# Optimization experiments

Hardware: AMD Instinct MI355X
Metric: run time of the kernel (lower is better)

## Reference

```python
import jax, jax.numpy as jnp
import numpy as np

TEMP = 0.5  # init temperature
EPS = 1e-12  # F.normalize eps


def setup_inputs() -> dict:
    key = jax.random.key(0)
    k1, k2 = jax.random.split(key)
    batch_embedding = jax.random.normal(k1, (4096, 256), dtype=jnp.float32)
    labels = jax.random.randint(k2, (4096,), 0, 512, dtype=jnp.int64)
    return {"batch_embedding": batch_embedding, "labels": labels}


def reference(batch_embedding, labels):
    n = labels.shape[0]
    dt = batch_embedding.dtype
    # row-normalize; cosine_similarity of normalized rows == norm @ norm.T
    nrm = jnp.linalg.norm(batch_embedding, axis=1, keepdims=True)
    norm = batch_embedding / jnp.maximum(nrm, EPS)
    sim = norm @ norm.T  # [n, n]
    mask = (labels[:, None] == labels[None, :]).astype(dt)  # same-label pairs (incl. diagonal)
    eye = jnp.eye(n, dtype=dt)
    exp_sim = jnp.exp(sim / TEMP) * (1.0 - eye)  # zero diagonal
    pos = mask * exp_sim
    neg_sum = jnp.sum(exp_sim - pos, axis=1)  # per-row negative sum
    ratio = pos / (pos + neg_sum[:, None])
    loss_mat = -jnp.log((1.0 - mask) + ratio + eye)
    nnz = jnp.count_nonzero(loss_mat).astype(dt)
    return jnp.sum(loss_mat) / nnz
```

## Files before the change

### kernel.cpp

```cpp
#include <hip/hip_runtime.h>
#include <hip/hip_bf16.h>


#define N_ROWS 4096
#define K_DIM  256

typedef __attribute__((ext_vector_type(4))) float float4v;
typedef __attribute__((ext_vector_type(4))) float f4;
typedef __attribute__((ext_vector_type(4))) int   int4v;
typedef __attribute__((ext_vector_type(2))) long  long2v;

#define PK_OFF    0
#define PART_OFF  (2 * 1024 * 1024)
#define ACC_OFF   (PART_OFF + 4 * 64 * N_ROWS * 4)

__device__ __forceinline__ void gll16(const void* g, void* l) {
    __builtin_amdgcn_global_load_lds(
        (const __attribute__((address_space(1))) unsigned int*)g,
        (__attribute__((address_space(3))) unsigned int*)l, 16, 0, 0);
}

__global__ void normalize_kernel(const float* __restrict__ emb,
                                 unsigned char* __restrict__ pk8,
                                 float* __restrict__ acc) {
    int tile = blockIdx.x, t = threadIdx.x;
    __shared__ float lds[16 * 256];
    __shared__ float sc[16];
    const f4* src = (const f4*)(emb + tile * 16 * 256);
    f4* dst4 = (f4*)lds;
    #pragma unroll
    for (int it = 0; it < 4; ++it) dst4[t + 256 * it] = src[t + 256 * it];
    __syncthreads();
    int wave = t >> 6, lane = t & 63;
    int row = wave * 4 + (lane >> 4);
    float s = 0.f;
    #pragma unroll
    for (int m = 0; m < 16; ++m) {
        float x = lds[row * 256 + (lane & 15) + 16 * m];
        s += x * x;
    }
    s += __shfl_xor(s, 1); s += __shfl_xor(s, 2);
    s += __shfl_xor(s, 4); s += __shfl_xor(s, 8);
    float scale = 1.0f / fmaxf(sqrtf(s), 1e-12f);
    if ((lane & 15) == 0) sc[row] = scale;
    __syncthreads();
    int u = t >> 6, quad = (t >> 4) & 3, r16 = t & 15;
    float s8 = sc[r16] * 8.0f;
    const float* lr = lds + r16 * 256;
    int4v wv;
    #pragma unroll
    for (int wi = 0; wi < 4; ++wi) {
        int h  = wi >> 1;
        int j0 = (wi & 1) * 4;
        int kb = quad * 8 + (2 * u + h) * 32 + j0;
        float v0 = lr[kb + 0] * s8, v1 = lr[kb + 1] * s8;
        float v2 = lr[kb + 2] * s8, v3 = lr[kb + 3] * s8;
        int wd = __builtin_amdgcn_cvt_pk_fp8_f32(v0, v1, 0, 0);
        wd     = __builtin_amdgcn_cvt_pk_fp8_f32(v2, v3, wd, 1);
        wv[wi] = wd;
    }
    *(int4v*)(pk8 + tile * 4096 + t * 16) = wv;
    if (tile == 0 && t < 4) acc[t] = 0.0f;
}

__global__ __launch_bounds__(256, 3)
void negsum_kernel(const unsigned char* __restrict__ pk8,
                   const int* __restrict__ labels,
                   float* __restrict__ part) {
    __shared__ __align__(16) unsigned char Bs8[32768];
    int t = threadIdx.x;
    int w = t >> 6, lane = t & 63;
    int lane16 = lane & 15, quad = lane >> 4;
    int xcd = blockIdx.x & 7, local = blockIdx.x >> 3;
    int bi = xcd * 4 + (local >> 5);
    int bj = local & 31;
    int wi = w >> 1, wj = w & 1;

    int ibase = bi * 128 + wi * 64;
    int jbase = bj * 128 + wj * 64;
    const char* pkb = (const char*)pk8;

    #pragma unroll
    for (int u = 0; u < 8; ++u) {
        int c8 = w * 8 + u, tl = c8 >> 2, cs = c8 & 3;
        gll16(pkb + (((bj * 8 + tl) << 12) | (cs << 10)) + lane * 16,
              Bs8 + (c8 << 10));
    }
    long2v av[4][4];
    #pragma unroll
    for (int it = 0; it < 4; ++it)
        #pragma unroll
        for (int cs = 0; cs < 4; ++cs)
            av[it][cs] = *(const long2v*)(pkb
                + (((bi * 8 + wi * 4 + it) << 12) | (cs << 10)) + lane * 16);

    int labi[16], labj[4];
    #pragma unroll
    for (int it = 0; it < 4; ++it)
        #pragma unroll
        for (int r = 0; r < 4; ++r)
            labi[it * 4 + r] = labels[ibase + it * 16 + quad * 4 + r];
    #pragma unroll
    for (int jt = 0; jt < 4; ++jt)
        labj[jt] = labels[jbase + jt * 16 + lane16];

    float4v acc[4][4];
    #pragma unroll
    for (int a = 0; a < 4; ++a)
        #pragma unroll
        for (int b = 0; b < 4; ++b)
            acc[a][b] = (float4v){0.f, 0.f, 0.f, 0.f};

    __syncthreads();

    #pragma unroll
    for (int cs = 0; cs < 4; ++cs) {
        long2v bv[4];
        #pragma unroll
        for (int jt = 0; jt < 4; ++jt)
            bv[jt] = *(const long2v*)(Bs8
                     + (((((wj * 4 + jt) << 2) | cs) << 10)) + lane * 16);
        #pragma unroll
        for (int h = 0; h < 2; ++h)
            #pragma unroll
            for (int it = 0; it < 4; ++it)
                #pragma unroll
                for (int jt = 0; jt < 4; ++jt)
                    acc[it][jt] = __builtin_amdgcn_mfma_f32_16x16x32_fp8_fp8(
                        av[it][cs][h], bv[jt][h], acc[it][jt], 0, 0, 0);
    }

    float ex[4] = {0,0,0,0}, pe[4] = {0,0,0,0};
    float tt[4] = {0,0,0,0}, pc[4] = {0,0,0,0};
    #pragma unroll
    for (int it = 0; it < 4; ++it) {
        #pragma unroll
        for (int jt = 0; jt < 4; ++jt) {
            int j = jbase + jt * 16 + lane16;
            #pragma unroll
            for (int r = 0; r < 4; ++r) {
                int i = ibase + it * 16 + quad * 4 + r;
                float t2 = acc[it][jt][r] * 0.03125f;
                float e  = __expf(t2);
                bool keep = (i != j);
                bool same = (labi[it * 4 + r] == labj[jt]);
                ex[jt] += keep ? e : 0.0f;
                float m = (same && keep) ? 1.0f : 0.0f;
                pe[jt] = fmaf(m, e,  pe[jt]);
                tt[jt] = fmaf(m, t2, tt[jt]);
                pc[jt] += m;
            }
        }
    }
    int i64 = bi * 2 + wi;
    #pragma unroll
    for (int jt = 0; jt < 4; ++jt) {
        float v0 = ex[jt], v1 = pe[jt], v2 = tt[jt], v3 = pc[jt];
        v0 += __shfl_xor(v0, 16); v0 += __shfl_xor(v0, 32);
        v1 += __shfl_xor(v1, 16); v1 += __shfl_xor(v1, 32);
        v2 += __shfl_xor(v2, 16); v2 += __shfl_xor(v2, 32);
        v3 += __shfl_xor(v3, 16); v3 += __shfl_xor(v3, 32);
        if (quad == 0) {
            int col = jbase + jt * 16 + lane16;
            part[((0 * 64 + i64) << 12) + col] = v0;
            part[((1 * 64 + i64) << 12) + col] = v1;
            part[((2 * 64 + i64) << 12) + col] = v2;
            part[((3 * 64 + i64) << 12) + col] = v3;
        }
    }
}

__global__ void rowreduce_kernel(const float* __restrict__ part,
                                 float* __restrict__ acc,
                                 float* __restrict__ out) {
    int t = threadIdx.x;
    int rl = t & 31, sl = t >> 5;
    int row = blockIdx.x * 32 + rl;
    float s[4];
    #pragma unroll
    for (int st = 0; st < 4; ++st) {
        float v = 0.f;
        #pragma unroll
        for (int c = 0; c < 8; ++c)
            v += part[((st * 64 + (sl * 8 + c)) << 12) + row];
        s[st] = v;
    }
    #pragma unroll
    for (int st = 0; st < 4; ++st) s[st] += __shfl_xor(s[st], 32);
    __shared__ float sred[4][4][32];
    int wave = t >> 6, lane = t & 63;
    if (lane < 32) {
        #pragma unroll
        for (int st = 0; st < 4; ++st) sred[wave][st][lane] = s[st];
    }
    __syncthreads();
    float lsum = 0.f, pcm = 0.f;
    if (t < 32) {
        float tot[4];
        #pragma unroll
        for (int st = 0; st < 4; ++st)
            tot[st] = sred[0][st][t] + sred[1][st][t]
                    + sred[2][st][t] + sred[3][st][t];
        if (tot[3] > 0.f) {
            float n = tot[0] - tot[1];
            lsum = tot[3] * logf(n) + tot[1] / n - tot[2];
            pcm  = tot[3];
        }
    }
    #pragma unroll
    for (int m = 1; m < 32; m <<= 1) {
        lsum += __shfl_xor(lsum, m);
        pcm  += __shfl_xor(pcm,  m);
    }
    if (t == 0) {
        atomicAdd(&acc[0], lsum);
        atomicAdd(&acc[1], pcm);
        __threadfence();
        int ticket = atomicAdd((int*)(acc + 2), 1);
        if (ticket == 127) {
            float ls = atomicAdd(&acc[0], 0.0f);
            float cs = atomicAdd(&acc[1], 0.0f);
            out[0] = ls / cs;
        }
    }
}

extern "C" void kernel_launch(void* const* d_in, const int* in_sizes, int n_in,
                              void* d_out, int out_size, void* d_ws, size_t ws_size,
                              hipStream_t stream) {
    const float* emb    = (const float*)d_in[0];
    const int*   labels = (const int*)d_in[1];
    float* out = (float*)d_out;
    char*  ws  = (char*)d_ws;

    unsigned char* pk8  = (unsigned char*)(ws + PK_OFF);
    float*         part = (float*)(ws + PART_OFF);
    float*         acc  = (float*)(ws + ACC_OFF);

    normalize_kernel<<<N_ROWS / 16, 256, 0, stream>>>(emb, pk8, acc);
    negsum_kernel<<<1024, 256, 0, stream>>>(pk8, labels, part);
    rowreduce_kernel<<<128, 256, 0, stream>>>(part, acc, out);
}
```

Baseline: 78.52 us.

## Process two column tiles per block and correct diagonal terms in row reduction

Each negsum block now handles two adjacent 128-column tiles, which halves the grid and reuses the A fragments held in registers. The second B tile is loaded into LDS while the first tile's epilogue runs. The per-element diagonal masking is removed from the epilogue. The row reduction instead subtracts the known diagonal contribution (exp(2), 2 and a count of 1), which assumes the diagonal similarity is exactly 1. Under fp8 quantization that self-similarity is only approximately 1, so the result can drift slightly.

```diff
diff --git a/kernel.cpp b/kernel.cpp
--- a/kernel.cpp
+++ b/kernel.cpp
@@ -72,18 +72,18 @@
     int w = t >> 6, lane = t & 63;
     int lane16 = lane & 15, quad = lane >> 4;
     int xcd = blockIdx.x & 7, local = blockIdx.x >> 3;
-    int bi = xcd * 4 + (local >> 5);
-    int bj = local & 31;
+    int bi  = xcd * 4 + (local >> 4);
+    int bjp = local & 15;
+    int bj0 = bjp * 2;
     int wi = w >> 1, wj = w & 1;
 
     int ibase = bi * 128 + wi * 64;
-    int jbase = bj * 128 + wj * 64;
     const char* pkb = (const char*)pk8;
 
     #pragma unroll
     for (int u = 0; u < 8; ++u) {
         int c8 = w * 8 + u, tl = c8 >> 2, cs = c8 & 3;
-        gll16(pkb + (((bj * 8 + tl) << 12) | (cs << 10)) + lane * 16,
+        gll16(pkb + (((bj0 * 8 + tl) << 12) | (cs << 10)) + lane * 16,
               Bs8 + (c8 << 10));
     }
     long2v av[4][4];
@@ -94,80 +94,99 @@
             av[it][cs] = *(const long2v*)(pkb
                 + (((bi * 8 + wi * 4 + it) << 12) | (cs << 10)) + lane * 16);
 
-    int labi[16], labj[4];
+    int labi[16], labj0[4], labj1[4];
     #pragma unroll
     for (int it = 0; it < 4; ++it)
         #pragma unroll
         for (int r = 0; r < 4; ++r)
             labi[it * 4 + r] = labels[ibase + it * 16 + quad * 4 + r];
     #pragma unroll
-    for (int jt = 0; jt < 4; ++jt)
-        labj[jt] = labels[jbase + jt * 16 + lane16];
+    for (int jt = 0; jt < 4; ++jt) {
+        labj0[jt] = labels[bj0 * 128       + wj * 64 + jt * 16 + lane16];
+        labj1[jt] = labels[bj0 * 128 + 128 + wj * 64 + jt * 16 + lane16];
+    }
 
     float4v acc[4][4];
+    int i64 = bi * 2 + wi;
+
+    auto mfma_tile = [&]() {
+        #pragma unroll
+        for (int cs = 0; cs < 4; ++cs) {
+            long2v bv[4];
+            #pragma unroll
+            for (int jt = 0; jt < 4; ++jt)
+                bv[jt] = *(const long2v*)(Bs8
+                         + (((((wj * 4 + jt) << 2) | cs) << 10)) + lane * 16);
+            #pragma unroll
+            for (int h = 0; h < 2; ++h)
+                #pragma unroll
+                for (int it = 0; it < 4; ++it)
+                    #pragma unroll
+                    for (int jt = 0; jt < 4; ++jt)
+                        acc[it][jt] = __builtin_amdgcn_mfma_f32_16x16x32_fp8_fp8(
+                            av[it][cs][h], bv[jt][h], acc[it][jt], 0, 0, 0);
+        }
+    };
+
+    auto epi_tile = [&](int jbase, const int (&labjl)[4]) {
+        float ex[4] = {0,0,0,0}, pe[4] = {0,0,0,0};
+        float tt[4] = {0,0,0,0}, pc[4] = {0,0,0,0};
+        #pragma unroll
+        for (int it = 0; it < 4; ++it) {
+            #pragma unroll
+            for (int jt = 0; jt < 4; ++jt) {
+                #pragma unroll
+                for (int r = 0; r < 4; ++r) {
+                    float t2 = acc[it][jt][r] * 0.03125f;
+                    float e  = __expf(t2);
+                    float m  = (labi[it * 4 + r] == labjl[jt]) ? 1.0f : 0.0f;
+                    ex[jt] += e;
+                    pe[jt] = fmaf(m, e,  pe[jt]);
+                    tt[jt] = fmaf(m, t2, tt[jt]);
+                    pc[jt] += m;
+                }
+            }
+        }
+        #pragma unroll
+        for (int jt = 0; jt < 4; ++jt) {
+            float v0 = ex[jt], v1 = pe[jt], v2 = tt[jt], v3 = pc[jt];
+            v0 += __shfl_xor(v0, 16); v0 += __shfl_xor(v0, 32);
+            v1 += __shfl_xor(v1, 16); v1 += __shfl_xor(v1, 32);
+            v2 += __shfl_xor(v2, 16); v2 += __shfl_xor(v2, 32);
+            v3 += __shfl_xor(v3, 16); v3 += __shfl_xor(v3, 32);
+            if (quad == 0) {
+                int col = jbase + jt * 16 + lane16;
+                part[((0 * 64 + i64) << 12) + col] = v0;
+                part[((1 * 64 + i64) << 12) + col] = v1;
+                part[((2 * 64 + i64) << 12) + col] = v2;
+                part[((3 * 64 + i64) << 12) + col] = v3;
+            }
+        }
+    };
+
     #pragma unroll
     for (int a = 0; a < 4; ++a)
         #pragma unroll
         for (int b = 0; b < 4; ++b)
             acc[a][b] = (float4v){0.f, 0.f, 0.f, 0.f};
-
-    __syncthreads();
-
-    #pragma unroll
-    for (int cs = 0; cs < 4; ++cs) {
-        long2v bv[4];
-        #pragma unroll
-        for (int jt = 0; jt < 4; ++jt)
-            bv[jt] = *(const long2v*)(Bs8
-                     + (((((wj * 4 + jt) << 2) | cs) << 10)) + lane * 16);
-        #pragma unroll
-        for (int h = 0; h < 2; ++h)
-            #pragma unroll
-            for (int it = 0; it < 4; ++it)
-                #pragma unroll
-                for (int jt = 0; jt < 4; ++jt)
-                    acc[it][jt] = __builtin_amdgcn_mfma_f32_16x16x32_fp8_fp8(
-                        av[it][cs][h], bv[jt][h], acc[it][jt], 0, 0, 0);
-    }
-
-    float ex[4] = {0,0,0,0}, pe[4] = {0,0,0,0};
-    float tt[4] = {0,0,0,0}, pc[4] = {0,0,0,0};
-    #pragma unroll
-    for (int it = 0; it < 4; ++it) {
-        #pragma unroll
-        for (int jt = 0; jt < 4; ++jt) {
-            int j = jbase + jt * 16 + lane16;
-            #pragma unroll
-            for (int r = 0; r < 4; ++r) {
-                int i = ibase + it * 16 + quad * 4 + r;
-                float t2 = acc[it][jt][r] * 0.03125f;
-                float e  = __expf(t2);
-                bool keep = (i != j);
-                bool same = (labi[it * 4 + r] == labj[jt]);
-                ex[jt] += keep ? e : 0.0f;
-                float m = (same && keep) ? 1.0f : 0.0f;
-                pe[jt] = fmaf(m, e,  pe[jt]);
-                tt[jt] = fmaf(m, t2, tt[jt]);
-                pc[jt] += m;
-            }
-        }
-    }
-    int i64 = bi * 2 + wi;
-    #pragma unroll
-    for (int jt = 0; jt < 4; ++jt) {
-        float v0 = ex[jt], v1 = pe[jt], v2 = tt[jt], v3 = pc[jt];
-        v0 += __shfl_xor(v0, 16); v0 += __shfl_xor(v0, 32);
-        v1 += __shfl_xor(v1, 16); v1 += __shfl_xor(v1, 32);
-        v2 += __shfl_xor(v2, 16); v2 += __shfl_xor(v2, 32);
-        v3 += __shfl_xor(v3, 16); v3 += __shfl_xor(v3, 32);
-        if (quad == 0) {
-            int col = jbase + jt * 16 + lane16;
-            part[((0 * 64 + i64) << 12) + col] = v0;
-            part[((1 * 64 + i64) << 12) + col] = v1;
-            part[((2 * 64 + i64) << 12) + col] = v2;
-            part[((3 * 64 + i64) << 12) + col] = v3;
-        }
-    }
+    __syncthreads();
+    mfma_tile();
+    __syncthreads();
+    #pragma unroll
+    for (int u = 0; u < 8; ++u) {
+        int c8 = w * 8 + u, tl = c8 >> 2, cs = c8 & 3;
+        gll16(pkb + ((((bj0 + 1) * 8 + tl) << 12) | (cs << 10)) + lane * 16,
+              Bs8 + (c8 << 10));
+    }
+    epi_tile(bj0 * 128 + wj * 64, labj0);
+    #pragma unroll
+    for (int a = 0; a < 4; ++a)
+        #pragma unroll
+        for (int b = 0; b < 4; ++b)
+            acc[a][b] = (float4v){0.f, 0.f, 0.f, 0.f};
+    __syncthreads();
+    mfma_tile();
+    epi_tile(bj0 * 128 + 128 + wj * 64, labj1);
 }
 
 __global__ void rowreduce_kernel(const float* __restrict__ part,
@@ -201,10 +220,13 @@
         for (int st = 0; st < 4; ++st)
             tot[st] = sred[0][st][t] + sred[1][st][t]
                     + sred[2][st][t] + sred[3][st][t];
-        if (tot[3] > 0.f) {
-            float n = tot[0] - tot[1];
-            lsum = tot[3] * logf(n) + tot[1] / n - tot[2];
-            pcm  = tot[3];
+        float n   = tot[0] - tot[1];
+        float pec = tot[1] - 7.3890560989f;
+        float ttc = tot[2] - 2.0f;
+        float pcc = tot[3] - 1.0f;
+        if (pcc > 0.5f) {
+            lsum = pcc * logf(n) + pec / n - ttc;
+            pcm  = pcc;
         }
     }
     #pragma unroll
@@ -238,6 +260,6 @@
     float*         acc  = (float*)(ws + ACC_OFF);
 
     normalize_kernel<<<N_ROWS / 16, 256, 0, stream>>>(emb, pk8, acc);
-    negsum_kernel<<<1024, 256, 0, stream>>>(pk8, labels, part);
+    negsum_kernel<<<512, 256, 0, stream>>>(pk8, labels, part);
     rowreduce_kernel<<<128, 256, 0, stream>>>(part, acc, out);
 }
```

Result: slower. 84.46 us (+7.6%).
